# Kernel optimization log

Measured on AMD Instinct MI355X. Metric: run time of the kernel, lower is better.

Reference implementation:

```python
import jax, jax.numpy as jnp
import numpy as np

SR_CUT = 10.0
N_ATOMS = 10000
N_PAIRS = 250000
K = 128          # radial basis size
H = 128          # interaction / output hidden width
NB = 5           # num_blocks
NIL = 2          # num_interaction_layers
NOL = 2          # num_output_layers
NO = 2           # num_outputs


def setup_inputs() -> dict:
    key = jax.random.key(0)
    ks = jax.random.split(key, 10)
    Z = jax.random.randint(ks[0], (N_ATOMS,), 0, 95)
    R = jax.random.normal(ks[1], (N_ATOMS, 3), dtype=jnp.float32) * 3.0
    idx_i = jnp.sort(jax.random.randint(ks[2], (N_PAIRS,), 0, N_ATOMS))
    idx_j = jax.random.randint(ks[3], (N_PAIRS,), 0, N_ATOMS)
    s = 0.05
    iW = jax.random.normal(ks[4], (NB, NIL, H, H), dtype=jnp.float32) * s
    iB = jnp.zeros((NB, NIL, H), dtype=jnp.float32)
    oW = jax.random.normal(ks[5], (NB, NOL, H, H), dtype=jnp.float32) * s
    oB = jnp.zeros((NB, NOL, H), dtype=jnp.float32)
    oWf = jax.random.normal(ks[6], (NB, H, NO), dtype=jnp.float32) * s
    oBf = jnp.zeros((NB, NO), dtype=jnp.float32)
    scales = jnp.ones((NO, 95), dtype=jnp.float32)
    shifts = jnp.zeros((NO, 95), dtype=jnp.float32)
    return {"Z": Z, "R": R, "idx_i": idx_i, "idx_j": idx_j,
            "iW": iW, "iB": iB, "oW": oW, "oB": oB,
            "oWf": oWf, "oBf": oBf, "scales": scales, "shifts": shifts}


def _ssp(x):
    # shifted softplus: softplus(x) - log(2)
    return jax.nn.softplus(x) - jnp.log(2.0).astype(x.dtype)


def _basis(rij):
    # smooth polynomial cutoff + Gaussian basis on exp(-r) (PhysNet-style 'Default' radial basis)
    x = rij / SR_CUT
    fcut = jnp.where(rij < SR_CUT, 1.0 - 6.0 * x**5 + 15.0 * x**4 - 10.0 * x**3, 0.0)
    mu = jnp.linspace(np.exp(-SR_CUT), 1.0, K, dtype=rij.dtype)          # [K]
    width = ((2.0 / K) * (1.0 - np.exp(-SR_CUT))) ** (-2)
    er = jnp.exp(-rij)[:, None]                                          # [P,1]
    return fcut[:, None] * jnp.exp(-width * (er - mu) ** 2)              # [P,K]


def reference(Z, R, idx_i, idx_j, iW, iB, oW, oB, oWf, oBf, scales, shifts):
    # pairwise distances via gather (bf_layer.getPairs)
    D = R[idx_j] - R[idx_i]                                              # [P,3]
    rij = jnp.sqrt(jnp.sum(D * D, axis=-1) + 1e-12)                      # [P]
    bf = _basis(rij)                                                     # [P,K]

    x = bf
    outputs = jnp.zeros((N_ATOMS, NO), dtype=R.dtype)
    nhloss = jnp.zeros((), dtype=R.dtype)
    lastout2 = None
    for b in range(NB):
        # interaction block: per-edge MLP (K==H so stacked weights are uniform)
        for l in range(NIL):
            x = _ssp(x @ iW[b, l] + iB[b, l])
        # output block: per-edge MLP + final linear head
        y = x
        for l in range(NOL):
            y = _ssp(y @ oW[b, l] + oB[b, l])
        out_e = y @ oWf[b] + oBf[b]                                      # [P,NO]
        out = jax.ops.segment_sum(out_e, idx_i, num_segments=N_ATOMS)    # [N,NO]
        outputs = outputs + out
        out2 = out ** 2
        if b > 0:
            nhloss = nhloss + jnp.mean(out2 / (out2 + lastout2 + 1e-7))
        lastout2 = out2

    sc = scales[:, Z].T                                                  # [N,NO]
    sh = shifts[:, Z].T                                                  # [N,NO]
    outputs = outputs * sc + sh
    return outputs, rij, nhloss
```

## Files before the change

kernel.cpp:

```cpp
#include <hip/hip_runtime.h>
#include <stdint.h>

#define NP   250000
#define NA   10000
#define NBLK 5
#define NL   20
#define BLOB_W_BYTES 16384
#define BLOB_BYTES   16896

#define LOG2E 1.4426950408889634f
#define LN2   0.6931471805599453f

typedef float  f32x4  __attribute__((ext_vector_type(4)));
typedef unsigned short ushort_t;
typedef unsigned int   uint_t;
typedef int4  i4_ma __attribute__((may_alias));
typedef uint2 u2_ma __attribute__((may_alias));
typedef uint_t u1_ma __attribute__((may_alias));

#if __has_builtin(__builtin_amdgcn_exp2f)
#define FEXP2(x) __builtin_amdgcn_exp2f(x)
#else
#define FEXP2(x) exp2f(x)
#endif
#if __has_builtin(__builtin_amdgcn_logf)
#define FLOG2(x) __builtin_amdgcn_logf(x)
#else
#define FLOG2(x) log2f(x)
#endif

__device__ uint8_t g_blob[NL * BLOB_BYTES];
__device__ float   g_outs[NBLK * NA * 2];
__device__ float   g_nh[1];
__device__ unsigned g_done;
__device__ float   g_Rf[NA * 3];
__device__ float   g_oWfF[NBLK * 128 * 2];
__device__ float   g_oBfF[NBLK * 2];
__device__ float   g_scF[190];
__device__ float   g_shF[190];

static __device__ __forceinline__ float bf2f(ushort_t u) {
    return __uint_as_float(((uint_t)u) << 16);
}
static __device__ uint8_t f2fp8(float f) {
    uint_t u = __float_as_uint(f);
    uint8_t s = (uint8_t)((u >> 24) & 0x80);
    float af = fabsf(f);
    if (af != af) return (uint8_t)(s | 0x7F);
    if (af > 448.0f) return (uint8_t)(s | 0x7E);
    int e = (int)((u >> 23) & 0xFF) - 127;
    uint_t m = u & 0x7FFFFFu;
    if (e >= -6) {
        uint_t mant = m >> 20;
        uint_t rest = m & 0xFFFFFu;
        if (rest > 0x80000u || (rest == 0x80000u && (mant & 1u))) mant++;
        uint_t ee = (uint_t)(e + 7);
        if (mant == 8u) { mant = 0u; ee++; }
        if (ee > 15u || (ee == 15u && mant > 6u)) return (uint8_t)(s | 0x7E);
        return (uint8_t)(s | (ee << 3) | mant);
    }
    int qq = (int)rintf(af * 512.0f);
    if (qq > 7) return (uint8_t)(s | 0x08);
    return (uint8_t)(s | (uint_t)qq);
}
template <bool HI>
static __device__ __forceinline__ int cvtpk2(float a, float b, int old) {
#if __has_builtin(__builtin_amdgcn_cvt_pk_fp8_f32)
    return __builtin_amdgcn_cvt_pk_fp8_f32(a, b, old, HI);
#else
    int p = (int)f2fp8(a) | ((int)f2fp8(b) << 8);
    return HI ? (int)((old & 0x0000FFFF) | ((uint_t)p << 16))
              : (int)((old & 0xFFFF0000) | (uint_t)p);
#endif
}
static __device__ __forceinline__ long u2l(u2_ma v) {
    union { u2_ma u; long l; } x; x.u = v; return x.l;
}
static __device__ __forceinline__ float ssp_u(float accv) {
    return FLOG2(0.5f + FEXP2(accv));
}

static __device__ __forceinline__ bool detect_is_f32(const ushort_t* probe) {
    __shared__ int flag;
    if (threadIdx.x == 0) flag = 0;
    __syncthreads();
    if (threadIdx.x < 256) {
        float v = fabsf(bf2f(probe[2 * threadIdx.x]));
        if (!(v <= 64.0f)) flag = 1;
    }
    __syncthreads();
    return flag != 0;
}
static __device__ __forceinline__ float in_elt(const void* p, int i, bool isf32) {
    return isf32 ? ((const float*)p)[i] : bf2f(((const ushort_t*)p)[i]);
}

__global__ void prep_kernel(const void* __restrict__ iW, const void* __restrict__ iB,
                            const void* __restrict__ oW, const void* __restrict__ oB,
                            const void* __restrict__ R, const void* __restrict__ oWf,
                            const void* __restrict__ oBf, const void* __restrict__ scales,
                            const void* __restrict__ shifts)
{
    const bool isf32 = detect_is_f32((const ushort_t*)iW);
    if (blockIdx.x < 80) {
        const int L = blockIdx.x >> 2;
        const int qr = blockIdx.x & 3;
        const int b = L >> 2, li = L & 3;
        const void* srcW = (li < 2) ? iW : oW;
        const void* srcB = (li < 2) ? iB : oB;
        const int lyr = (li < 2) ? (b * 2 + li) : (b * 2 + li - 2);
        const int wofs = lyr * 16384;
        const int bofs = lyr * 128;
        uint8_t* blob = g_blob + (size_t)L * BLOB_BYTES;
        uint_t* dw = (uint_t*)blob;
        float*  db = (float*)(blob + BLOB_W_BYTES);
        const float sc = (L == 0) ? LOG2E : 1.0f;
        for (int t = threadIdx.x; t < 1024; t += blockDim.x) {
            int d = qr * 1024 + t;
            int n = d & 127, kg = d >> 7;
            float w0 = sc * in_elt(srcW, wofs + (kg * 4 + 0) * 128 + n, isf32);
            float w1 = sc * in_elt(srcW, wofs + (kg * 4 + 1) * 128 + n, isf32);
            float w2 = sc * in_elt(srcW, wofs + (kg * 4 + 2) * 128 + n, isf32);
            float w3 = sc * in_elt(srcW, wofs + (kg * 4 + 3) * 128 + n, isf32);
            int w = cvtpk2<false>(w0, w1, 0);
            w = cvtpk2<true>(w2, w3, w);
            dw[n * 32 + 2 * ((kg >> 1) ^ (n & 15)) + (kg & 1)] = (uint_t)w;
        }
        if (qr == 0)
            for (int m = threadIdx.x; m < 128; m += blockDim.x)
                db[m] = in_elt(srcB, bofs + m, isf32) * LOG2E - 1.0f;
    } else {
        const int t = (blockIdx.x - 80) * 256 + threadIdx.x;
        if (t < NBLK * NA * 2) g_outs[t] = 0.0f;
        if (t == 0) { g_nh[0] = 0.0f; g_done = 0u; }
        if (t < NA * 3)      g_Rf[t]   = in_elt(R, t, isf32);
        if (t < NBLK * 256)  g_oWfF[t] = LN2 * in_elt(oWf, t, isf32);
        if (t < NBLK * 2)    g_oBfF[t] = in_elt(oBf, t, isf32);
        if (t < 190)         g_scF[t]  = in_elt(scales, t, isf32);
        if (t < 190)         g_shF[t]  = in_elt(shifts, t, isf32);
    }
}

__global__ __launch_bounds__(256, 3)
void pairs_mlp_kernel(const int* __restrict__ idx_i,
                      const int* __restrict__ idx_j,
                      float* __restrict__ out_rij)
{
    __shared__ i4_ma w_lds[2048];
    __shared__ u2_ma act_all[4 * 512];

    const i4_ma* gW0 = (const i4_ma*)g_blob;
    i4_ma s0 = gW0[threadIdx.x];
    i4_ma s1 = gW0[threadIdx.x + 256];
    i4_ma s2 = gW0[threadIdx.x + 512];
    i4_ma s3 = gW0[threadIdx.x + 768];

    const int wave = threadIdx.x >> 6;
    const int lane = threadIdx.x & 63;
    u2_ma* act = act_all + wave * 512;

    const int pp = lane & 31;
    const int p0 = blockIdx.x * 128 + wave * 32;
    const int p = p0 + pp;
    const bool valid = (p < NP);

    int ai = 0, aj = 0;
    if (valid) { ai = idx_i[p]; aj = idx_j[p]; }
    float xi0 = g_Rf[3 * ai + 0], xi1 = g_Rf[3 * ai + 1], xi2 = g_Rf[3 * ai + 2];
    float xj0 = g_Rf[3 * aj + 0], xj1 = g_Rf[3 * aj + 1], xj2 = g_Rf[3 * aj + 2];
    float dx = xj0 - xi0, dy = xj1 - xi1, dz = xj2 - xi2;
    float rij = sqrtf(dx * dx + dy * dy + dz * dz + 1e-12f);
    if (lane < 32 && valid) out_rij[p] = rij;

    float fcut = 0.0f;
    if (valid && rij < 10.0f) {
        float xc = rij * 0.1f;
        float x3 = xc * xc * xc;
        fcut = 1.0f + x3 * (-10.0f + xc * (15.0f - 6.0f * xc));
    }
    const float mu0 = 4.5399929762484854e-05f;
    const float dmu = (1.0f - mu0) / 127.0f;
    const float wc = (2.0f / 128.0f) * (1.0f - mu0);
    const float NW2 = -(1.0f / (wc * wc)) * LOG2E;
    float er = FEXP2(-rij * LOG2E);

    const int q = lane >> 4;
    const int l15 = lane & 15;
    const int aseg = valid ? ai : -1;

    u2_ma bfrX[2][4];
    {
        float er_n[2], fc_n[2];
        er_n[0] = __shfl(er, l15, 64);      fc_n[0] = __shfl(fcut, l15, 64);
        er_n[1] = __shfl(er, 16 + l15, 64); fc_n[1] = __shfl(fcut, 16 + l15, 64);
#pragma unroll
        for (int nt = 0; nt < 2; ++nt)
#pragma unroll
            for (int kt = 0; kt < 4; ++kt) {
                float v[8];
#pragma unroll
                for (int jj = 0; jj < 8; ++jj) {
                    int g = kt * 32 + q * 8 + jj;
                    float mu = mu0 + (float)g * dmu;
                    float e0 = er_n[nt] - mu;
                    v[jj] = fc_n[nt] * FEXP2(NW2 * e0 * e0);
                }
                int w0 = cvtpk2<false>(v[0], v[1], 0);
                w0 = cvtpk2<true>(v[2], v[3], w0);
                int w1 = cvtpk2<false>(v[4], v[5], 0);
                w1 = cvtpk2<true>(v[6], v[7], w1);
                bfrX[nt][kt].x = (uint_t)w0;
                bfrX[nt][kt].y = (uint_t)w1;
            }
    }

    w_lds[threadIdx.x]       = s0;
    w_lds[threadIdx.x + 256] = s1;
    w_lds[threadIdx.x + 512] = s2;
    w_lds[threadIdx.x + 768] = s3;
    __syncthreads();

    for (int blk = 0; blk < NBLK; ++blk) {
#pragma unroll
        for (int li = 0; li < 4; ++li) {
            const int L = blk * 4 + li;
            const bool hasNext = (L + 1 < NL);

            i4_ma pf0, pf1, pf2, pf3;
            if (hasNext) {
                const i4_ma* gWn = (const i4_ma*)(g_blob + (size_t)(L + 1) * BLOB_BYTES);
                pf0 = gWn[threadIdx.x];
                pf1 = gWn[threadIdx.x + 256];
                pf2 = gWn[threadIdx.x + 512];
                pf3 = gWn[threadIdx.x + 768];
            }

            const u2_ma* wl2 = (const u2_ma*)(w_lds + (li & 1) * 1024);
            const float* bb = (const float*)(g_blob + (size_t)L * BLOB_BYTES + BLOB_W_BYTES);

            f32x4 bias[8];
#pragma unroll
            for (int mt = 0; mt < 8; ++mt)
                bias[mt] = *(const f32x4*)(bb + mt * 16 + q * 4);

            f32x4 acc[2][8];
#pragma unroll
            for (int kt = 0; kt < 4; ++kt) {
                const int cc = kt * 4 + q;
                u2_ma b0, b1;
                if (li == 0) {
                    b0 = bfrX[0][kt];
                    b1 = bfrX[1][kt];
                } else {
                    b0 = act[(l15) * 16 + (cc ^ l15)];
                    b1 = act[(16 + l15) * 16 + (cc ^ l15)];
                    if (li == 2) { bfrX[0][kt] = b0; bfrX[1][kt] = b1; }
                }
                const long lb0 = u2l(b0), lb1 = u2l(b1);
#pragma unroll
                for (int mt = 0; mt < 8; ++mt) {
                    const long la = u2l(wl2[(mt * 16 + l15) * 16 + (cc ^ l15)]);
                    acc[0][mt] = __builtin_amdgcn_mfma_f32_16x16x32_fp8_fp8(
                        la, lb0, (kt == 0) ? bias[mt] : acc[0][mt], 0, 0, 0);
                    acc[1][mt] = __builtin_amdgcn_mfma_f32_16x16x32_fp8_fp8(
                        la, lb1, (kt == 0) ? bias[mt] : acc[1][mt], 0, 0, 0);
                }
            }

            if (li < 3) {
#pragma unroll
                for (int mt = 0; mt < 8; ++mt) {
                    const int c = mt * 2 + (q >> 1);
#pragma unroll
                    for (int nt = 0; nt < 2; ++nt) {
                        float u0 = ssp_u(acc[nt][mt][0]);
                        float u1 = ssp_u(acc[nt][mt][1]);
                        float u2 = ssp_u(acc[nt][mt][2]);
                        float u3 = ssp_u(acc[nt][mt][3]);
                        int w = cvtpk2<false>(u0, u1, 0);
                        w = cvtpk2<true>(u2, u3, w);
                        const int rp = nt * 16 + l15;
                        ((u1_ma*)&act[rp * 16 + (c ^ (rp & 15))])[q & 1] = (uint_t)w;
                    }
                }
            } else {
                const float* hw = g_oWfF + blk * 256;
                const float ob0 = g_oBfF[blk * 2 + 0];
                const float ob1 = g_oBfF[blk * 2 + 1];
                float hs[2][2];
#pragma unroll
                for (int nt = 0; nt < 2; ++nt) {
                    float h0 = 0.f, h1 = 0.f;
#pragma unroll
                    for (int mt = 0; mt < 8; ++mt) {
#pragma unroll
                        for (int rr = 0; rr < 4; ++rr) {
                            float u = ssp_u(acc[nt][mt][rr]);
                            const int f = mt * 16 + q * 4 + rr;
                            h0 = fmaf(u, hw[f * 2 + 0], h0);
                            h1 = fmaf(u, hw[f * 2 + 1], h1);
                        }
                    }
                    h0 += __shfl_xor(h0, 16, 64);
                    h0 += __shfl_xor(h0, 32, 64);
                    h1 += __shfl_xor(h1, 16, 64);
                    h1 += __shfl_xor(h1, 32, 64);
                    hs[nt][0] = h0; hs[nt][1] = h1;
                }
                float c0v = (pp < 16) ? hs[0][0] : hs[1][0];
                float c1v = (pp < 16) ? hs[0][1] : hs[1][1];
                c0v += ob0; c1v += ob1;
#pragma unroll
                for (int d = 1; d < 32; d <<= 1) {
                    float t0 = __shfl_up(c0v, d, 64);
                    float t1 = __shfl_up(c1v, d, 64);
                    int   an = __shfl_up(aseg, d, 64);
                    if (pp >= d && an == aseg) { c0v += t0; c1v += t1; }
                }
                int ain = __shfl_down(aseg, 1, 64);
                bool tail = (pp == 31) || (ain != aseg);
                if (lane < 32 && valid && tail) {
                    atomicAdd(&g_outs[(blk * NA + aseg) * 2 + 0], c0v);
                    atomicAdd(&g_outs[(blk * NA + aseg) * 2 + 1], c1v);
                }
            }

            if (hasNext) {
                i4_ma* dstb = w_lds + ((li + 1) & 1) * 1024;
                dstb[threadIdx.x]       = pf0;
                dstb[threadIdx.x + 256] = pf1;
                dstb[threadIdx.x + 512] = pf2;
                dstb[threadIdx.x + 768] = pf3;
                __syncthreads();
            }
        }
    }
}

__global__ void finalize_kernel(const int* __restrict__ Z,
                                float* __restrict__ out_atoms,
                                float* __restrict__ out_nh)
{
    __shared__ float red[256];
    const int a = blockIdx.x * 256 + threadIdx.x;
    float s = 0.f;
    if (a < NA) {
        float v[NBLK][2];
        float t0 = 0.f, t1 = 0.f;
#pragma unroll
        for (int b = 0; b < NBLK; ++b) {
            v[b][0] = g_outs[(b * NA + a) * 2 + 0];
            v[b][1] = g_outs[(b * NA + a) * 2 + 1];
            t0 += v[b][0]; t1 += v[b][1];
        }
        const int z = Z[a];
        out_atoms[a * 2 + 0] = t0 * g_scF[z]      + g_shF[z];
        out_atoms[a * 2 + 1] = t1 * g_scF[95 + z] + g_shF[95 + z];
#pragma unroll
        for (int b = 1; b < NBLK; ++b)
#pragma unroll
            for (int o = 0; o < 2; ++o) {
                float x2 = v[b][o] * v[b][o];
                float p2 = v[b - 1][o] * v[b - 1][o];
                s += x2 / (x2 + p2 + 1e-7f);
            }
    }
    red[threadIdx.x] = s;
    __syncthreads();
    for (int st = 128; st > 0; st >>= 1) {
        if (threadIdx.x < st) red[threadIdx.x] += red[threadIdx.x + st];
        __syncthreads();
    }
    if (threadIdx.x == 0) {
        atomicAdd(&g_nh[0], red[0]);
        __threadfence();
        unsigned old = atomicAdd(&g_done, 1u);
        if (old == gridDim.x - 1) {
            float v = atomicAdd(&g_nh[0], 0.0f);
            out_nh[0] = v * (1.0f / 20000.0f);
        }
    }
}

extern "C" void kernel_launch(void* const* d_in, const int* in_sizes, int n_in,
                              void* d_out, int out_size, void* d_ws, size_t ws_size,
                              hipStream_t stream)
{
    const int* Z     = (const int*)d_in[0];
    const void* R    = d_in[1];
    const int* idx_i = (const int*)d_in[2];
    const int* idx_j = (const int*)d_in[3];
    const void* iW   = d_in[4];
    const void* iB   = d_in[5];
    const void* oW   = d_in[6];
    const void* oB   = d_in[7];
    const void* oWf  = d_in[8];
    const void* oBf  = d_in[9];
    const void* scales = d_in[10];
    const void* shifts = d_in[11];

    float* out_f = (float*)d_out;

    prep_kernel<<<80 + 391, 256, 0, stream>>>(iW, iB, oW, oB, R, oWf, oBf, scales, shifts);
    pairs_mlp_kernel<<<(NP + 127) / 128, 256, 0, stream>>>(idx_i, idx_j, out_f + 2 * NA);
    finalize_kernel<<<(NA + 255) / 256, 256, 0, stream>>>(Z, out_f, out_f + 2 * NA + NP);
}
```

Before: 289.0 us.

## Replace double-buffered weight prefetch with single-buffer synchronous loads

Removes the register-held prefetch of the next layer's weights and the LDS double buffer. Each layer now loads its weights directly into a single LDS buffer between two barriers, and initializes the accumulators from the bias instead of selecting per MFMA. This halves weight LDS use and cuts register pressure, which may allow more resident blocks. The cost is that global weight loads are no longer overlapped with compute and an extra barrier is added per layer.

```diff
diff --git a/kernel.cpp b/kernel.cpp
--- a/kernel.cpp
+++ b/kernel.cpp
@@ -146,18 +146,13 @@
                       const int* __restrict__ idx_j,
                       float* __restrict__ out_rij)
 {
-    __shared__ i4_ma w_lds[2048];
+    __shared__ i4_ma w_lds[1024];
     __shared__ u2_ma act_all[4 * 512];
-
-    const i4_ma* gW0 = (const i4_ma*)g_blob;
-    i4_ma s0 = gW0[threadIdx.x];
-    i4_ma s1 = gW0[threadIdx.x + 256];
-    i4_ma s2 = gW0[threadIdx.x + 512];
-    i4_ma s3 = gW0[threadIdx.x + 768];
 
     const int wave = threadIdx.x >> 6;
     const int lane = threadIdx.x & 63;
     u2_ma* act = act_all + wave * 512;
+    const u2_ma* wl2 = (const u2_ma*)w_lds;
 
     const int pp = lane & 31;
     const int p0 = blockIdx.x * 128 + wave * 32;
@@ -214,36 +209,26 @@
             }
     }
 
-    w_lds[threadIdx.x]       = s0;
-    w_lds[threadIdx.x + 256] = s1;
-    w_lds[threadIdx.x + 512] = s2;
-    w_lds[threadIdx.x + 768] = s3;
-    __syncthreads();
-
     for (int blk = 0; blk < NBLK; ++blk) {
 #pragma unroll
         for (int li = 0; li < 4; ++li) {
             const int L = blk * 4 + li;
-            const bool hasNext = (L + 1 < NL);
-
-            i4_ma pf0, pf1, pf2, pf3;
-            if (hasNext) {
-                const i4_ma* gWn = (const i4_ma*)(g_blob + (size_t)(L + 1) * BLOB_BYTES);
-                pf0 = gWn[threadIdx.x];
-                pf1 = gWn[threadIdx.x + 256];
-                pf2 = gWn[threadIdx.x + 512];
-                pf3 = gWn[threadIdx.x + 768];
-            }
-
-            const u2_ma* wl2 = (const u2_ma*)(w_lds + (li & 1) * 1024);
+            const i4_ma* gW = (const i4_ma*)(g_blob + (size_t)L * BLOB_BYTES);
             const float* bb = (const float*)(g_blob + (size_t)L * BLOB_BYTES + BLOB_W_BYTES);
 
-            f32x4 bias[8];
-#pragma unroll
-            for (int mt = 0; mt < 8; ++mt)
-                bias[mt] = *(const f32x4*)(bb + mt * 16 + q * 4);
+            __syncthreads();
+#pragma unroll
+            for (int it = 0; it < 4; ++it)
+                w_lds[threadIdx.x + it * 256] = gW[threadIdx.x + it * 256];
+            __syncthreads();
 
             f32x4 acc[2][8];
+#pragma unroll
+            for (int mt = 0; mt < 8; ++mt) {
+                const f32x4 bias = *(const f32x4*)(bb + mt * 16 + q * 4);
+                acc[0][mt] = bias;
+                acc[1][mt] = bias;
+            }
 #pragma unroll
             for (int kt = 0; kt < 4; ++kt) {
                 const int cc = kt * 4 + q;
@@ -261,9 +246,9 @@
                 for (int mt = 0; mt < 8; ++mt) {
                     const long la = u2l(wl2[(mt * 16 + l15) * 16 + (cc ^ l15)]);
                     acc[0][mt] = __builtin_amdgcn_mfma_f32_16x16x32_fp8_fp8(
-                        la, lb0, (kt == 0) ? bias[mt] : acc[0][mt], 0, 0, 0);
+                        la, lb0, acc[0][mt], 0, 0, 0);
                     acc[1][mt] = __builtin_amdgcn_mfma_f32_16x16x32_fp8_fp8(
-                        la, lb1, (kt == 0) ? bias[mt] : acc[1][mt], 0, 0, 0);
+                        la, lb1, acc[1][mt], 0, 0, 0);
                 }
             }
 
@@ -323,15 +308,6 @@
                     atomicAdd(&g_outs[(blk * NA + aseg) * 2 + 0], c0v);
                     atomicAdd(&g_outs[(blk * NA + aseg) * 2 + 1], c1v);
                 }
-            }
-
-            if (hasNext) {
-                i4_ma* dstb = w_lds + ((li + 1) & 1) * 1024;
-                dstb[threadIdx.x]       = pf0;
-                dstb[threadIdx.x + 256] = pf1;
-                dstb[threadIdx.x + 512] = pf2;
-                dstb[threadIdx.x + 768] = pf3;
-                __syncthreads();
             }
         }
     }
```

After: 268.0 us. -7.3%, faster.
